# Optimization experiments

Hardware: AMD Instinct MI355X
Metric: run time of the kernel (lower is better)

The kernel has to match this reference:

```python
import jax, jax.numpy as jnp
import numpy as np
import math

NUM_BUCKETS = 32
MAX_DISTANCE = 128
N_HEADS = 16
D_KV = 64


def _relative_position_bucket(relative_position, num_buckets=NUM_BUCKETS, max_distance=MAX_DISTANCE):
    # bidirectional (encoder) variant: is_decoder=False
    nb = num_buckets // 2
    rel_buckets = (relative_position > 0).astype(jnp.int32) * nb
    rp = jnp.abs(relative_position)
    max_exact = nb // 2
    is_small = rp < max_exact
    rp_large = max_exact + (
        jnp.log(rp.astype(jnp.float32) / max_exact)
        / math.log(max_distance / max_exact)
        * (nb - max_exact)
    ).astype(jnp.int32)
    rp_large = jnp.minimum(rp_large, nb - 1)
    return rel_buckets + jnp.where(is_small, rp, rp_large)


def compute_position_bias(rel_bias_table, q_len, k_len):
    ctx = jnp.arange(q_len, dtype=jnp.int32)[:, None]
    mem = jnp.arange(k_len, dtype=jnp.int32)[None, :]
    buckets = _relative_position_bucket(mem - ctx)  # [q_len, k_len]
    values = rel_bias_table[buckets]                # [q_len, k_len, H]
    return jnp.transpose(values, (2, 0, 1))[None]   # [1, H, q_len, k_len]


def setup_inputs() -> dict:
    key = jax.random.key(0)
    ks = jax.random.split(key, 6)
    B, S, D = 2, 2048, 1024
    s = 0.02
    return {
        "hidden_states": jax.random.normal(ks[0], (B, S, D), dtype=jnp.float32),
        "Wq": jax.random.normal(ks[1], (D, N_HEADS * D_KV), dtype=jnp.float32) * s,
        "Wk": jax.random.normal(ks[2], (D, N_HEADS * D_KV), dtype=jnp.float32) * s,
        "Wv": jax.random.normal(ks[3], (D, N_HEADS * D_KV), dtype=jnp.float32) * s,
        "Wo": jax.random.normal(ks[4], (N_HEADS * D_KV, D), dtype=jnp.float32) * s,
        "rel_bias_table": jax.random.normal(ks[5], (NUM_BUCKETS, N_HEADS), dtype=jnp.float32),
    }


def reference(hidden_states, Wq, Wk, Wv, Wo, rel_bias_table):
    B, S, D = hidden_states.shape
    H, dh = N_HEADS, D_KV
    q = (hidden_states @ Wq).reshape(B, S, H, dh)
    k = (hidden_states @ Wk).reshape(B, S, H, dh)
    v = (hidden_states @ Wv).reshape(B, S, H, dh)

    position_bias = compute_position_bias(rel_bias_table, S, S)  # [1,H,S,S]

    scale = 1.0 / math.sqrt(dh)  # applied inside optimized_attention (SDPA convention)
    scores = jnp.einsum('bqhd,bkhd->bhqk', q, k) * scale + position_bias
    probs = jax.nn.softmax(scores, axis=-1)
    ctx = jnp.einsum('bhqk,bkhd->bqhd', probs, v).reshape(B, S, H * dh)
    attn_output = ctx @ Wo
    return attn_output
```

## Files before the change

### kernel.cpp

```cpp
#include <hip/hip_runtime.h>

typedef __attribute__((ext_vector_type(8))) short s16x8;
typedef __attribute__((ext_vector_type(4))) float f32x4;
typedef unsigned short u16;
typedef unsigned int u32;

#define LOG2E 1.4426950408889634f

__device__ __forceinline__ u16 f2bf(float x) {
  u32 u = __float_as_uint(x);
  u += 0x7FFFu + ((u >> 16) & 1u);
  return (u16)(u >> 16);
}

__device__ __forceinline__ void gl_lds16(const void* g, void* l) {
  __builtin_amdgcn_global_load_lds((const __attribute__((address_space(1))) void*)g,
                                   (__attribute__((address_space(3))) void*)l, 16, 0, 0);
}

#define MFMA16(a, b, c) __builtin_amdgcn_mfma_f32_16x16x32_bf16((a), (b), (c), 0, 0, 0)


__global__ __launch_bounds__(256) void cast_hs(const float* __restrict__ src,
                                               u16* __restrict__ dst) {
  const int i = blockIdx.x * 256 + threadIdx.x;
  const float4* s4 = (const float4*)src;
  float4 a = s4[i * 2];
  float4 b = s4[i * 2 + 1];
  s16x8 o;
  o[0] = (short)f2bf(a.x); o[1] = (short)f2bf(a.y);
  o[2] = (short)f2bf(a.z); o[3] = (short)f2bf(a.w);
  o[4] = (short)f2bf(b.x); o[5] = (short)f2bf(b.y);
  o[6] = (short)f2bf(b.z); o[7] = (short)f2bf(b.w);
  *(s16x8*)&dst[i * 8] = o;
}

__global__ __launch_bounds__(256) void wtrans(const float* __restrict__ W,
                                              u16* __restrict__ Wt) {
  const int t = threadIdx.x;
  const int n = blockIdx.x * 64 + (t & 63);
  const int kb = blockIdx.y * 32 + (t >> 6) * 8;
  s16x8 o;
#pragma unroll
  for (int j = 0; j < 8; ++j) o[j] = (short)f2bf(W[(kb + j) * 1024 + n]);
  *(s16x8*)&Wt[n * 1024 + kb] = o;
}

__global__ __launch_bounds__(256) void bias_table(const float* __restrict__ tbl,
                                                  float* __restrict__ biasT) {
  const int i = blockIdx.x * 256 + threadIdx.x;
  const int h = i >> 12, dp = i & 4095;
  const int delta = dp - 2047;
  const int rp = delta < 0 ? -delta : delta;
  int bucket = delta > 0 ? 16 : 0;
  if (rp < 8)
    bucket += rp;
  else
    bucket += 8 + (rp >= 12) + (rp >= 16) + (rp >= 23) + (rp >= 32) +
              (rp >= 46) + (rp >= 64) + (rp >= 91);
  biasT[i] = tbl[bucket * 16 + h] * LOG2E;
}

__global__ __launch_bounds__(256) void vtrans(const u16* __restrict__ V,
                                              u16* __restrict__ VT) {
  const int tid = threadIdx.x;
  const int bh = blockIdx.y;
  const int b = bh >> 4, h = bh & 15;
  const int s0 = blockIdx.x * 32;
  const int d = tid & 63;
  const int si = tid >> 6;
  s16x8 o;
#pragma unroll
  for (int j = 0; j < 8; ++j)
    o[j] = (short)V[(b * 2048 + s0 + si * 8 + j) * 1024 + h * 64 + d];
  *(s16x8*)&VT[(bh * 64 + d) * 2048 + s0 + si * 8] = o;
}


__device__ __forceinline__ void gemm_core(const u16* __restrict__ A,
                                          const u16* __restrict__ Bt,
                                          int m0, int n0,
                                          u16* As, u16* Bs, f32x4 acc[4][4]) {
  const int tid = threadIdx.x;
  const int w = tid >> 6, l = tid & 63, g = l >> 4, m15 = l & 15;
  const int wr = (w >> 1) * 64, wc = (w & 1) * 64;
#pragma unroll
  for (int i = 0; i < 4; ++i)
#pragma unroll
    for (int j = 0; j < 4; ++j) acc[i][j] = (f32x4){0.f, 0.f, 0.f, 0.f};

  for (int kt = 0; kt < 16; ++kt) {
    const int k0 = kt * 64;
    __syncthreads();
#pragma unroll
    for (int c = 0; c < 4; ++c) {
      const int idx = c * 256 + tid;
      const int row = idx >> 3, col16 = idx & 7;
      const int scol = col16 ^ (row & 7);
      gl_lds16(&A[(m0 + row) * 1024 + k0 + scol * 8], (char*)As + c * 4096 + w * 1024);
      gl_lds16(&Bt[(n0 + row) * 1024 + k0 + scol * 8], (char*)Bs + c * 4096 + w * 1024);
    }
    __syncthreads();
#pragma unroll
    for (int ks = 0; ks < 2; ++ks) {
      s16x8 af[4], bf[4];
#pragma unroll
      for (int mf = 0; mf < 4; ++mf) {
        const int row = wr + mf * 16 + m15;
        af[mf] = *(const s16x8*)&As[(row * 8 + ((ks * 4 + g) ^ (row & 7))) * 8];
      }
#pragma unroll
      for (int nf = 0; nf < 4; ++nf) {
        const int row = wc + nf * 16 + m15;
        bf[nf] = *(const s16x8*)&Bs[(row * 8 + ((ks * 4 + g) ^ (row & 7))) * 8];
      }
#pragma unroll
      for (int mf = 0; mf < 4; ++mf)
#pragma unroll
        for (int nf = 0; nf < 4; ++nf)
          acc[mf][nf] = MFMA16(af[mf], bf[nf], acc[mf][nf]);
    }
  }
}

__global__ __launch_bounds__(256) void gemm_qkv(const u16* __restrict__ X,
                                                const u16* __restrict__ Wt,
                                                u16* __restrict__ Q,
                                                u16* __restrict__ Kb,
                                                u16* __restrict__ Vb) {
  __shared__ u16 As[8192], Bs[8192];
  f32x4 acc[4][4];
  const int m0 = blockIdx.x * 128, n0 = blockIdx.y * 128;
  gemm_core(X, Wt, m0, n0, As, Bs, acc);

  const int tid = threadIdx.x;
  const int w = tid >> 6, l = tid & 63, g = l >> 4, m15 = l & 15;
  const int wr = (w >> 1) * 64, wc = (w & 1) * 64;
  const int nsel = n0 >> 10;
  u16* dst = nsel == 0 ? Q : (nsel == 1 ? Kb : Vb);
  const float scale = nsel == 0 ? 0.125f * LOG2E : 1.0f;
  const int ncol0 = (n0 & 1023) + wc;
#pragma unroll
  for (int mf = 0; mf < 4; ++mf) {
    const int rbase = m0 + wr + mf * 16 + g * 4;
#pragma unroll
    for (int nf = 0; nf < 4; ++nf) {
      const int col = ncol0 + nf * 16 + m15;
#pragma unroll
      for (int r = 0; r < 4; ++r)
        dst[(rbase + r) * 1024 + col] = f2bf(acc[mf][nf][r] * scale);
    }
  }
}

__global__ __launch_bounds__(256) void gemm_out(const u16* __restrict__ CTX,
                                                const u16* __restrict__ Wot,
                                                float* __restrict__ Out) {
  __shared__ u16 As[8192], Bs[8192];
  f32x4 acc[4][4];
  const int m0 = blockIdx.x * 128, n0 = blockIdx.y * 128;
  gemm_core(CTX, Wot, m0, n0, As, Bs, acc);

  const int tid = threadIdx.x;
  const int w = tid >> 6, l = tid & 63, g = l >> 4, m15 = l & 15;
  const int wr = (w >> 1) * 64, wc = (w & 1) * 64;
#pragma unroll
  for (int mf = 0; mf < 4; ++mf) {
    const int rbase = m0 + wr + mf * 16 + g * 4;
#pragma unroll
    for (int nf = 0; nf < 4; ++nf) {
      const int col = n0 + wc + nf * 16 + m15;
#pragma unroll
      for (int r = 0; r < 4; ++r)
        Out[(rbase + r) * 1024 + col] = acc[mf][nf][r];
    }
  }
}


__global__ __launch_bounds__(256) void attn_kernel(const u16* __restrict__ Qg,
                                                   const u16* __restrict__ Kg,
                                                   const u16* __restrict__ VTg,
                                                   const float* __restrict__ biasT,
                                                   const float* __restrict__ tbl,
                                                   u16* __restrict__ CTX) {
  __shared__ u16 KT[2][4096];
  __shared__ u16 VTs[2][4096];
  __shared__ u16 P[4][1024];

  const int tid = threadIdx.x;
  const int w = tid >> 6, l = tid & 63, g = l >> 4, m15 = l & 15;
  const int bh = blockIdx.y, b = bh >> 4, h = bh & 15;
  const int q0 = blockIdx.x * 64;

  const float fpos = tbl[31 * 16 + h] * LOG2E;
  const float fneg = tbl[15 * 16 + h] * LOG2E;

  const int qrow = q0 + w * 16 + m15;
  const u16* qp = &Qg[(b * 2048 + qrow) * 1024 + h * 64 + g * 8];
  const s16x8 aq0 = *(const s16x8*)qp;
  const s16x8 aq1 = *(const s16x8*)(qp + 32);

  s16x8 vone;
#pragma unroll
  for (int j = 0; j < 8; ++j) vone[j] = (short)0x3F80;

  f32x4 o[4];
  f32x4 ls4 = (f32x4){0.f, 0.f, 0.f, 0.f};
#pragma unroll
  for (int d = 0; d < 4; ++d) o[d] = (f32x4){0.f, 0.f, 0.f, 0.f};

  const int R0 = w * 16 + g * 4;
  u16* Pw = &P[w][0];

  const u16* Kbase = &Kg[(b * 2048) * 1024 + h * 64];
  const u16* Vbase = &VTg[bh * 64 * 2048];

#define STAGE(buf, kv0)                                                          \
  {                                                                              \
    _Pragma("unroll") for (int c = 0; c < 2; ++c) {                              \
      const int idx = c * 256 + tid;                                             \
      const int row = idx >> 3, col16 = idx & 7;                                 \
      const int scol = col16 ^ (row & 7);                                        \
      gl_lds16(&Kbase[(kv0 + row) * 1024 + scol * 8],                            \
               (char*)KT + (buf)*8192 + c * 4096 + w * 1024);                    \
      gl_lds16(&Vbase[row * 2048 + (kv0) + scol * 8],                            \
               (char*)VTs + (buf)*8192 + c * 4096 + w * 1024);                   \
    }                                                                            \
  }

  STAGE(0, 0);
  int cur = 0;
  for (int t = 0; t < 32; ++t) {
    const int kv0 = t * 64;
    __syncthreads();
    if (t < 31) STAGE(cur ^ 1, kv0 + 64);

    const u16* KTc = &KT[cur][0];
    const u16* VTc = &VTs[cur][0];

    f32x4 s[4];
    const int diff = kv0 - q0;
    if (diff >= 192 || diff <= -192) {
      const float bc = diff > 0 ? fpos : fneg;
#pragma unroll
      for (int c = 0; c < 4; ++c) s[c] = (f32x4){bc, bc, bc, bc};
    } else {
      const float* bp = &biasT[h * 4096 + kv0 + m15 - (q0 + R0) + 2047];
#pragma unroll
      for (int c = 0; c < 4; ++c)
#pragma unroll
        for (int r = 0; r < 4; ++r) s[c][r] = bp[c * 16 - r];
    }

#pragma unroll
    for (int ks = 0; ks < 2; ++ks) {
      const s16x8 a = ks ? aq1 : aq0;
#pragma unroll
      for (int c = 0; c < 4; ++c) {
        const int row = c * 16 + m15;
        const s16x8 bk = *(const s16x8*)&KTc[(row * 8 + ((ks * 4 + g) ^ (row & 7))) * 8];
        s[c] = MFMA16(a, bk, s[c]);
      }
    }

#pragma unroll
    for (int c = 0; c < 4; ++c) {
#pragma unroll
      for (int r = 0; r < 4; ++r) {
        const float p = __builtin_amdgcn_exp2f(s[c][r]);
        const int Rr = g * 4 + r;
        const int byt = Rr * 128 + (((c * 16 + m15) * 2) ^ ((Rr & 7) << 4));
        Pw[byt >> 1] = (u16)(__float_as_uint(p) >> 16);
      }
    }

#pragma unroll
    for (int ks = 0; ks < 2; ++ks) {
      const s16x8 pa =
          *(const s16x8*)&Pw[(m15 * 128 + ((ks * 64 + g * 16) ^ ((m15 & 7) << 4))) >> 1];
#pragma unroll
      for (int d = 0; d < 4; ++d) {
        const int rowv = d * 16 + m15;
        const s16x8 bv = *(const s16x8*)&VTc[(rowv * 8 + ((ks * 4 + g) ^ (rowv & 7))) * 8];
        o[d] = MFMA16(pa, bv, o[d]);
      }
      ls4 = MFMA16(pa, vone, ls4);
    }
    cur ^= 1;
  }
#undef STAGE

  f32x4 inv;
#pragma unroll
  for (int r = 0; r < 4; ++r) inv[r] = 1.0f / ls4[r];
  const int orow = b * 2048 + q0 + w * 16 + g * 4;
  const int ocol = h * 64 + m15;
#pragma unroll
  for (int d = 0; d < 4; ++d) {
#pragma unroll
    for (int r = 0; r < 4; ++r)
      CTX[(orow + r) * 1024 + ocol + d * 16] = f2bf(o[d][r] * inv[r]);
  }
}


extern "C" void kernel_launch(void* const* d_in, const int* in_sizes, int n_in,
                              void* d_out, int out_size, void* d_ws, size_t ws_size,
                              hipStream_t stream) {
  (void)in_sizes; (void)n_in; (void)out_size; (void)ws_size;
  const float* hs  = (const float*)d_in[0];
  const float* Wq  = (const float*)d_in[1];
  const float* Wk  = (const float*)d_in[2];
  const float* Wv  = (const float*)d_in[3];
  const float* Wo  = (const float*)d_in[4];
  const float* tbl = (const float*)d_in[5];

  char* ws = (char*)d_ws;
  u16* hsb   = (u16*)(ws);
  u16* wt    = (u16*)(ws + 8388608);
  u16* wot   = (u16*)(ws + 14680064);
  u16* q     = (u16*)(ws + 16777216);
  u16* k     = (u16*)(ws + 25165824);
  u16* v     = (u16*)(ws + 33554432);
  u16* vt    = (u16*)(ws + 41943040);
  u16* ctx   = (u16*)(ws + 50331648);
  float* biasT = (float*)(ws + 58720256);

  cast_hs<<<2048, 256, 0, stream>>>(hs, hsb);
  wtrans<<<dim3(16, 32), 256, 0, stream>>>(Wq, wt);
  wtrans<<<dim3(16, 32), 256, 0, stream>>>(Wk, wt + 1048576);
  wtrans<<<dim3(16, 32), 256, 0, stream>>>(Wv, wt + 2097152);
  wtrans<<<dim3(16, 32), 256, 0, stream>>>(Wo, wot);
  bias_table<<<256, 256, 0, stream>>>(tbl, biasT);
  gemm_qkv<<<dim3(32, 24), 256, 0, stream>>>(hsb, wt, q, k, v);
  vtrans<<<dim3(64, 32), 256, 0, stream>>>(v, vt);
  attn_kernel<<<dim3(32, 32), 256, 0, stream>>>(q, k, vt, biasT, tbl, ctx);
  gemm_out<<<dim3(32, 8), 256, 0, stream>>>(ctx, wot, (float*)d_out);
}
```

Before: 145.0 us.

## Fuse prep kernels, remap GEMM/attention grids, widen attention Q tile to 128

Merges the hidden-state cast, four weight transposes and bias-table build into one prep launch to cut launch overhead. GEMM and attention blocks are remapped through a flat index so that blocks sharing operands are spread across XCDs. The attention kernel now processes 32 query rows per wave (128 per block), reusing each K/V LDS tile for twice as many queries. It also computes S transposed so P can be stored as packed 8-byte writes. The larger tile raises register and LDS pressure and halves the grid to 512 blocks.

```diff
diff --git a/kernel.cpp b/kernel.cpp
--- a/kernel.cpp
+++ b/kernel.cpp
@@ -2,6 +2,7 @@
 
 typedef __attribute__((ext_vector_type(8))) short s16x8;
 typedef __attribute__((ext_vector_type(4))) float f32x4;
+typedef __attribute__((ext_vector_type(2))) unsigned int u32x2;
 typedef unsigned short u16;
 typedef unsigned int u32;
 
@@ -13,6 +14,10 @@
   return (u16)(u >> 16);
 }
 
+__device__ __forceinline__ u32 pack_bf_trunc(float lo, float hi) {
+  return (__float_as_uint(lo) >> 16) | (__float_as_uint(hi) & 0xFFFF0000u);
+}
+
 __device__ __forceinline__ void gl_lds16(const void* g, void* l) {
   __builtin_amdgcn_global_load_lds((const __attribute__((address_space(1))) void*)g,
                                    (__attribute__((address_space(3))) void*)l, 16, 0, 0);
@@ -21,44 +26,54 @@
 #define MFMA16(a, b, c) __builtin_amdgcn_mfma_f32_16x16x32_bf16((a), (b), (c), 0, 0, 0)
 
 
-__global__ __launch_bounds__(256) void cast_hs(const float* __restrict__ src,
-                                               u16* __restrict__ dst) {
-  const int i = blockIdx.x * 256 + threadIdx.x;
-  const float4* s4 = (const float4*)src;
-  float4 a = s4[i * 2];
-  float4 b = s4[i * 2 + 1];
-  s16x8 o;
-  o[0] = (short)f2bf(a.x); o[1] = (short)f2bf(a.y);
-  o[2] = (short)f2bf(a.z); o[3] = (short)f2bf(a.w);
-  o[4] = (short)f2bf(b.x); o[5] = (short)f2bf(b.y);
-  o[6] = (short)f2bf(b.z); o[7] = (short)f2bf(b.w);
-  *(s16x8*)&dst[i * 8] = o;
-}
-
-__global__ __launch_bounds__(256) void wtrans(const float* __restrict__ W,
-                                              u16* __restrict__ Wt) {
-  const int t = threadIdx.x;
-  const int n = blockIdx.x * 64 + (t & 63);
-  const int kb = blockIdx.y * 32 + (t >> 6) * 8;
-  s16x8 o;
-#pragma unroll
-  for (int j = 0; j < 8; ++j) o[j] = (short)f2bf(W[(kb + j) * 1024 + n]);
-  *(s16x8*)&Wt[n * 1024 + kb] = o;
-}
-
-__global__ __launch_bounds__(256) void bias_table(const float* __restrict__ tbl,
-                                                  float* __restrict__ biasT) {
-  const int i = blockIdx.x * 256 + threadIdx.x;
-  const int h = i >> 12, dp = i & 4095;
-  const int delta = dp - 2047;
-  const int rp = delta < 0 ? -delta : delta;
-  int bucket = delta > 0 ? 16 : 0;
-  if (rp < 8)
-    bucket += rp;
-  else
-    bucket += 8 + (rp >= 12) + (rp >= 16) + (rp >= 23) + (rp >= 32) +
-              (rp >= 46) + (rp >= 64) + (rp >= 91);
-  biasT[i] = tbl[bucket * 16 + h] * LOG2E;
+__global__ __launch_bounds__(256) void prep(const float* __restrict__ hs,
+                                            const float* __restrict__ Wq,
+                                            const float* __restrict__ Wk,
+                                            const float* __restrict__ Wv,
+                                            const float* __restrict__ Wo,
+                                            const float* __restrict__ tbl,
+                                            u16* __restrict__ hsb,
+                                            u16* __restrict__ wt,
+                                            u16* __restrict__ wot,
+                                            float* __restrict__ biasT) {
+  const int blk = blockIdx.x;
+  const int tid = threadIdx.x;
+  if (blk < 2048) {
+    const int i = blk * 256 + tid;
+    const float4* s4 = (const float4*)hs;
+    float4 a = s4[i * 2];
+    float4 b = s4[i * 2 + 1];
+    s16x8 o;
+    o[0] = (short)f2bf(a.x); o[1] = (short)f2bf(a.y);
+    o[2] = (short)f2bf(a.z); o[3] = (short)f2bf(a.w);
+    o[4] = (short)f2bf(b.x); o[5] = (short)f2bf(b.y);
+    o[6] = (short)f2bf(b.z); o[7] = (short)f2bf(b.w);
+    *(s16x8*)&hsb[i * 8] = o;
+  } else if (blk < 4096) {
+    int r = blk - 2048;
+    const int sel = r >> 9;
+    r &= 511;
+    const float* W = sel == 0 ? Wq : (sel == 1 ? Wk : (sel == 2 ? Wv : Wo));
+    u16* dst = sel == 3 ? wot : wt + sel * 1048576;
+    const int n = (r & 15) * 64 + (tid & 63);
+    const int kb = (r >> 4) * 32 + (tid >> 6) * 8;
+    s16x8 o;
+#pragma unroll
+    for (int j = 0; j < 8; ++j) o[j] = (short)f2bf(W[(kb + j) * 1024 + n]);
+    *(s16x8*)&dst[n * 1024 + kb] = o;
+  } else {
+    const int i = (blk - 4096) * 256 + tid;
+    const int h = i >> 12, dp = i & 4095;
+    const int delta = dp - 2047;
+    const int rp = delta < 0 ? -delta : delta;
+    int bucket = delta > 0 ? 16 : 0;
+    if (rp < 8)
+      bucket += rp;
+    else
+      bucket += 8 + (rp >= 12) + (rp >= 16) + (rp >= 23) + (rp >= 32) +
+                (rp >= 46) + (rp >= 64) + (rp >= 91);
+    biasT[i] = tbl[bucket * 16 + h] * LOG2E;
+  }
 }
 
 __global__ __launch_bounds__(256) void vtrans(const u16* __restrict__ V,
@@ -130,7 +145,10 @@
                                                 u16* __restrict__ Vb) {
   __shared__ u16 As[8192], Bs[8192];
   f32x4 acc[4][4];
-  const int m0 = blockIdx.x * 128, n0 = blockIdx.y * 128;
+  const int flat = blockIdx.x;
+  const int x = flat & 7, i = flat >> 3;
+  const int m0 = ((x & 3) * 8 + (i & 7)) * 128;
+  const int n0 = ((x >> 2) * 12 + (i >> 3)) * 128;
   gemm_core(X, Wt, m0, n0, As, Bs, acc);
 
   const int tid = threadIdx.x;
@@ -158,7 +176,10 @@
                                                 float* __restrict__ Out) {
   __shared__ u16 As[8192], Bs[8192];
   f32x4 acc[4][4];
-  const int m0 = blockIdx.x * 128, n0 = blockIdx.y * 128;
+  const int flat = blockIdx.x;
+  const int x = flat & 7, i = flat >> 3;
+  const int m0 = ((x & 3) * 8 + (i & 7)) * 128;
+  const int n0 = ((x >> 2) * 4 + (i >> 3)) * 128;
   gemm_core(CTX, Wot, m0, n0, As, Bs, acc);
 
   const int tid = threadIdx.x;
@@ -178,40 +199,50 @@
 }
 
 
-__global__ __launch_bounds__(256) void attn_kernel(const u16* __restrict__ Qg,
-                                                   const u16* __restrict__ Kg,
-                                                   const u16* __restrict__ VTg,
-                                                   const float* __restrict__ biasT,
-                                                   const float* __restrict__ tbl,
-                                                   u16* __restrict__ CTX) {
+__global__ __launch_bounds__(256, 2) void attn_kernel(const u16* __restrict__ Qg,
+                                                      const u16* __restrict__ Kg,
+                                                      const u16* __restrict__ VTg,
+                                                      const float* __restrict__ biasT,
+                                                      const float* __restrict__ tbl,
+                                                      u16* __restrict__ CTX) {
   __shared__ u16 KT[2][4096];
   __shared__ u16 VTs[2][4096];
-  __shared__ u16 P[4][1024];
+  __shared__ u16 P[4][2048];
 
   const int tid = threadIdx.x;
   const int w = tid >> 6, l = tid & 63, g = l >> 4, m15 = l & 15;
-  const int bh = blockIdx.y, b = bh >> 4, h = bh & 15;
-  const int q0 = blockIdx.x * 64;
+  const int flat = blockIdx.x;
+  const int nf_ = (flat & 7) * 64 + (flat >> 3);
+  const int qblk = nf_ & 15, bh = nf_ >> 4;
+  const int b = bh >> 4, h = bh & 15;
+  const int qw = qblk * 128 + w * 32;
 
   const float fpos = tbl[31 * 16 + h] * LOG2E;
   const float fneg = tbl[15 * 16 + h] * LOG2E;
 
-  const int qrow = q0 + w * 16 + m15;
-  const u16* qp = &Qg[(b * 2048 + qrow) * 1024 + h * 64 + g * 8];
-  const s16x8 aq0 = *(const s16x8*)qp;
-  const s16x8 aq1 = *(const s16x8*)(qp + 32);
+  s16x8 aq[2][2];
+#pragma unroll
+  for (int qs = 0; qs < 2; ++qs) {
+    const u16* qp = &Qg[(b * 2048 + qw + qs * 16 + m15) * 1024 + h * 64 + g * 8];
+    aq[qs][0] = *(const s16x8*)qp;
+    aq[qs][1] = *(const s16x8*)(qp + 32);
+  }
 
   s16x8 vone;
 #pragma unroll
   for (int j = 0; j < 8; ++j) vone[j] = (short)0x3F80;
 
-  f32x4 o[4];
-  f32x4 ls4 = (f32x4){0.f, 0.f, 0.f, 0.f};
-#pragma unroll
-  for (int d = 0; d < 4; ++d) o[d] = (f32x4){0.f, 0.f, 0.f, 0.f};
-
-  const int R0 = w * 16 + g * 4;
+  f32x4 o[2][4];
+  f32x4 ls4[2];
+#pragma unroll
+  for (int qs = 0; qs < 2; ++qs) {
+    ls4[qs] = (f32x4){0.f, 0.f, 0.f, 0.f};
+#pragma unroll
+    for (int d = 0; d < 4; ++d) o[qs][d] = (f32x4){0.f, 0.f, 0.f, 0.f};
+  }
+
   u16* Pw = &P[w][0];
+  const int pswz = (m15 & 7) << 4;
 
   const u16* Kbase = &Kg[(b * 2048) * 1024 + h * 64];
   const u16* Vbase = &VTg[bh * 64 * 2048];
@@ -239,68 +270,85 @@
     const u16* KTc = &KT[cur][0];
     const u16* VTc = &VTs[cur][0];
 
-    f32x4 s[4];
-    const int diff = kv0 - q0;
-    if (diff >= 192 || diff <= -192) {
+    f32x4 s[2][4];
+    const int diff = kv0 - qw;
+    if (diff <= -160 || diff >= 128) {
       const float bc = diff > 0 ? fpos : fneg;
 #pragma unroll
-      for (int c = 0; c < 4; ++c) s[c] = (f32x4){bc, bc, bc, bc};
+      for (int qs = 0; qs < 2; ++qs)
+#pragma unroll
+        for (int c = 0; c < 4; ++c) s[qs][c] = (f32x4){bc, bc, bc, bc};
     } else {
-      const float* bp = &biasT[h * 4096 + kv0 + m15 - (q0 + R0) + 2047];
-#pragma unroll
-      for (int c = 0; c < 4; ++c)
-#pragma unroll
-        for (int r = 0; r < 4; ++r) s[c][r] = bp[c * 16 - r];
+#pragma unroll
+      for (int qs = 0; qs < 2; ++qs) {
+        const float* bp = &biasT[h * 4096 + kv0 + g * 4 - qw - qs * 16 - m15 + 2047];
+#pragma unroll
+        for (int c = 0; c < 4; ++c)
+#pragma unroll
+          for (int r = 0; r < 4; ++r) s[qs][c][r] = bp[c * 16 + r];
+      }
     }
 
 #pragma unroll
     for (int ks = 0; ks < 2; ++ks) {
-      const s16x8 a = ks ? aq1 : aq0;
 #pragma unroll
       for (int c = 0; c < 4; ++c) {
         const int row = c * 16 + m15;
         const s16x8 bk = *(const s16x8*)&KTc[(row * 8 + ((ks * 4 + g) ^ (row & 7))) * 8];
-        s[c] = MFMA16(a, bk, s[c]);
-      }
-    }
-
-#pragma unroll
-    for (int c = 0; c < 4; ++c) {
-#pragma unroll
-      for (int r = 0; r < 4; ++r) {
-        const float p = __builtin_amdgcn_exp2f(s[c][r]);
-        const int Rr = g * 4 + r;
-        const int byt = Rr * 128 + (((c * 16 + m15) * 2) ^ ((Rr & 7) << 4));
-        Pw[byt >> 1] = (u16)(__float_as_uint(p) >> 16);
+        s[0][c] = MFMA16(bk, aq[0][ks], s[0][c]);
+        s[1][c] = MFMA16(bk, aq[1][ks], s[1][c]);
+      }
+    }
+
+#pragma unroll
+    for (int qs = 0; qs < 2; ++qs) {
+      const int q32 = qs * 16 + m15;
+#pragma unroll
+      for (int c = 0; c < 4; ++c) {
+        const u32 w0 = pack_bf_trunc(__builtin_amdgcn_exp2f(s[qs][c][0]),
+                                     __builtin_amdgcn_exp2f(s[qs][c][1]));
+        const u32 w1 = pack_bf_trunc(__builtin_amdgcn_exp2f(s[qs][c][2]),
+                                     __builtin_amdgcn_exp2f(s[qs][c][3]));
+        const int byt = q32 * 128 + c * 32 + g * 8;
+        *(u32x2*)((char*)Pw + (byt ^ pswz)) = (u32x2){w0, w1};
       }
     }
 
 #pragma unroll
     for (int ks = 0; ks < 2; ++ks) {
-      const s16x8 pa =
-          *(const s16x8*)&Pw[(m15 * 128 + ((ks * 64 + g * 16) ^ ((m15 & 7) << 4))) >> 1];
+      s16x8 pa[2];
+#pragma unroll
+      for (int qs = 0; qs < 2; ++qs) {
+        const int byt = (qs * 16 + m15) * 128 + ks * 64 + g * 16;
+        pa[qs] = *(const s16x8*)((const char*)Pw + (byt ^ pswz));
+      }
 #pragma unroll
       for (int d = 0; d < 4; ++d) {
         const int rowv = d * 16 + m15;
         const s16x8 bv = *(const s16x8*)&VTc[(rowv * 8 + ((ks * 4 + g) ^ (rowv & 7))) * 8];
-        o[d] = MFMA16(pa, bv, o[d]);
-      }
-      ls4 = MFMA16(pa, vone, ls4);
+        o[0][d] = MFMA16(pa[0], bv, o[0][d]);
+        o[1][d] = MFMA16(pa[1], bv, o[1][d]);
+      }
+      ls4[0] = MFMA16(pa[0], vone, ls4[0]);
+      ls4[1] = MFMA16(pa[1], vone, ls4[1]);
     }
     cur ^= 1;
   }
 #undef STAGE
 
-  f32x4 inv;
-#pragma unroll
-  for (int r = 0; r < 4; ++r) inv[r] = 1.0f / ls4[r];
-  const int orow = b * 2048 + q0 + w * 16 + g * 4;
-  const int ocol = h * 64 + m15;
-#pragma unroll
-  for (int d = 0; d < 4; ++d) {
-#pragma unroll
-    for (int r = 0; r < 4; ++r)
-      CTX[(orow + r) * 1024 + ocol + d * 16] = f2bf(o[d][r] * inv[r]);
+#pragma unroll
+  for (int qs = 0; qs < 2; ++qs) {
+    f32x4 inv;
+#pragma unroll
+    for (int r = 0; r < 4; ++r) inv[r] = 1.0f / ls4[qs][r];
+    const int orow = b * 2048 + qw + qs * 16 + g * 4;
+    const int ocol = h * 64 + m15;
+#pragma unroll
+    for (int d = 0; d < 4; ++d) {
+#pragma unroll
+      for (int r = 0; r < 4; ++r)
+        CTX[(orow + r) * 1024 + ocol + d * 16] = f2bf(o[qs][d][r] * inv[r]);
+    }
   }
 }
 
@@ -327,14 +375,9 @@
   u16* ctx   = (u16*)(ws + 50331648);
   float* biasT = (float*)(ws + 58720256);
 
-  cast_hs<<<2048, 256, 0, stream>>>(hs, hsb);
-  wtrans<<<dim3(16, 32), 256, 0, stream>>>(Wq, wt);
-  wtrans<<<dim3(16, 32), 256, 0, stream>>>(Wk, wt + 1048576);
-  wtrans<<<dim3(16, 32), 256, 0, stream>>>(Wv, wt + 2097152);
-  wtrans<<<dim3(16, 32), 256, 0, stream>>>(Wo, wot);
-  bias_table<<<256, 256, 0, stream>>>(tbl, biasT);
-  gemm_qkv<<<dim3(32, 24), 256, 0, stream>>>(hsb, wt, q, k, v);
+  prep<<<4352, 256, 0, stream>>>(hs, Wq, Wk, Wv, Wo, tbl, hsb, wt, wot, biasT);
+  gemm_qkv<<<768, 256, 0, stream>>>(hsb, wt, q, k, v);
   vtrans<<<dim3(64, 32), 256, 0, stream>>>(v, vt);
-  attn_kernel<<<dim3(32, 32), 256, 0, stream>>>(q, k, vt, biasT, tbl, ctx);
-  gemm_out<<<dim3(32, 8), 256, 0, stream>>>(ctx, wot, (float*)d_out);
-}
+  attn_kernel<<<512, 256, 0, stream>>>(q, k, vt, biasT, tbl, ctx);
+  gemm_out<<<256, 256, 0, stream>>>(ctx, wot, (float*)d_out);
+}
```

Measured after the change: 122.1 us. -15.8%, faster.
